# Performance work log

Measured on AMD Instinct MI355X. Metric: run time of the kernel, lower is better.

The kernel has to match this reference:

```python
import jax, jax.numpy as jnp
import numpy as np

D_MODEL = 1024
NUM_HEADS = 16
D_K = D_MODEL // NUM_HEADS


def setup_inputs() -> dict:
    key = jax.random.key(0)
    ks = jax.random.split(key, 11)
    B, S = 2, 2048
    s = 1.0 / np.sqrt(D_MODEL)
    inp = {
        'q': jax.random.normal(ks[0], (B, S, D_MODEL), jnp.float32),
        'k': jax.random.normal(ks[1], (B, S, D_MODEL), jnp.float32),
        'v': jax.random.normal(ks[2], (B, S, D_MODEL), jnp.float32),
        'w_q': jax.random.normal(ks[3], (D_MODEL, D_MODEL), jnp.float32) * s,
        'b_q': jnp.zeros((D_MODEL,), jnp.float32),
        'w_k': jax.random.normal(ks[4], (D_MODEL, D_MODEL), jnp.float32) * s,
        'b_k': jnp.zeros((D_MODEL,), jnp.float32),
        'w_v': jax.random.normal(ks[5], (D_MODEL, D_MODEL), jnp.float32) * s,
        'b_v': jnp.zeros((D_MODEL,), jnp.float32),
        'w_o': jax.random.normal(ks[6], (D_MODEL, D_MODEL), jnp.float32) * s,
        'b_o': jnp.zeros((D_MODEL,), jnp.float32),
    }
    return inp


def reference(q, k, v, w_q, b_q, w_k, b_k, w_v, b_v, w_o, b_o):
    B, S, _ = q.shape
    # linear projections (torch Linear: x @ W.T + b)
    def proj(x, w, b):
        y = x @ w.T + b
        # [B, S, D] -> [B, H, S, d_k]
        return y.reshape(B, -1, NUM_HEADS, D_K).transpose(0, 2, 1, 3)

    Q = proj(q, w_q, b_q)
    K = proj(k, w_k, b_k)
    V = proj(v, w_v, b_v)

    scale = 1.0 / np.sqrt(D_K).astype(np.float32)
    scores = jnp.einsum('bhqd,bhkd->bhqk', Q, K) * scale  # [B,H,S,S]
    weights = jax.nn.softmax(scores, axis=-1)
    # dropout is identity in eval mode
    x = jnp.einsum('bhqk,bhkd->bhqd', weights, V)
    x = x.transpose(0, 2, 1, 3).reshape(B, S, NUM_HEADS * D_K)
    return x @ w_o.T + b_o
```

## Files before the change

kernel.cpp:

```cpp
#include <hip/hip_runtime.h>

typedef __attribute__((ext_vector_type(8))) short short8;
typedef __attribute__((ext_vector_type(4))) float f32x4;

#define NHEADS 16
#define DK 64
#define SEQ 2048
#define DMODEL 1024

__device__ __forceinline__ unsigned short f2bf(float f) {
  union { float f; unsigned int u; } c; c.f = f;
  unsigned int u = c.u;
  return (unsigned short)((u + 0x7FFFu + ((u >> 16) & 1u)) >> 16);
}

__device__ __forceinline__ float exp2_hw(float x) {
  float y;
  asm("v_exp_f32 %0, %1" : "=v"(y) : "v"(x));
  return y;
}

__device__ __forceinline__ unsigned int cvtpk_bf16(float lo, float hi) {
  unsigned int r;
  asm("v_cvt_pk_bf16_f32 %0, %1, %2" : "=v"(r) : "v"(lo), "v"(hi));
  return r;
}

__device__ __forceinline__ short8 ldg16(const unsigned short* p) {
  return *reinterpret_cast<const short8*>(p);
}

__device__ __forceinline__ void gload_lds16(const unsigned short* g, unsigned short* l) {
  __builtin_amdgcn_global_load_lds(
      (const __attribute__((address_space(1))) unsigned int*)g,
      (__attribute__((address_space(3))) unsigned int*)l, 16, 0, 0);
}

struct CastPtrs {
  const float* s0; const float* s1; const float* s2; const float* s3;
  const float* s4; const float* s5; const float* s6;
  unsigned short* d0; unsigned short* d1; unsigned short* d2; unsigned short* d3;
  unsigned short* d4; unsigned short* d5; unsigned short* d6;
};

__global__ void cast_all(CastPtrs c) {
  const int b = blockIdx.x;
  const float* s; unsigned short* d; int off;
  if (b < 4096)        { s = c.s0; d = c.d0; off = b; }
  else if (b < 8192)   { s = c.s1; d = c.d1; off = b - 4096; }
  else if (b < 12288)  { s = c.s2; d = c.d2; off = b - 8192; }
  else if (b < 13312)  { s = c.s3; d = c.d3; off = b - 12288; }
  else if (b < 14336)  { s = c.s4; d = c.d4; off = b - 13312; }
  else if (b < 15360)  { s = c.s5; d = c.d5; off = b - 14336; }
  else                 { s = c.s6; d = c.d6; off = b - 15360; }
  const int i = off * 256 + threadIdx.x;
  float4 v = reinterpret_cast<const float4*>(s)[i];
  ushort4 o;
  o.x = f2bf(v.x); o.y = f2bf(v.y); o.z = f2bf(v.z); o.w = f2bf(v.w);
  reinterpret_cast<ushort4*>(d)[i] = o;
}

struct ProjPtrs {
  const unsigned short* A0; const unsigned short* A1; const unsigned short* A2;
  const unsigned short* W0; const unsigned short* W1; const unsigned short* W2;
  const float* bias0; const float* bias1; const float* bias2;
  unsigned short* dst0; unsigned short* dst1; unsigned short* dst2;
};

__global__ __launch_bounds__(256) void gemm_proj(ProjPtrs p) {
  __shared__ __align__(16) unsigned short S[24576];
  const int mode = blockIdx.z;
  const unsigned short* A = mode == 0 ? p.A0 : (mode == 1 ? p.A1 : p.A2);
  const unsigned short* W = mode == 0 ? p.W0 : (mode == 1 ? p.W1 : p.W2);
  const float* bias = mode == 0 ? p.bias0 : (mode == 1 ? p.bias1 : p.bias2);
  unsigned short* dst = mode == 0 ? p.dst0 : (mode == 1 ? p.dst1 : p.dst2);
  const int m0 = blockIdx.y * 128, n0 = blockIdx.x * 128;
  const int t = threadIdx.x, lane = t & 63, w = t >> 6;
  const int wr = w >> 1, wc = w & 1;
  const int lr = lane >> 4, lc = lane & 15;
  const unsigned short* a_src0 = A + (size_t)(m0 + (t >> 2)) * DMODEL + (t & 3) * 8;
  const unsigned short* a_src1 = a_src0 + (size_t)64 * DMODEL;
  const unsigned short* w_src0 = W + (size_t)(n0 + (t >> 2)) * DMODEL + (t & 3) * 8;
  const unsigned short* w_src1 = w_src0 + (size_t)64 * DMODEL;

  f32x4 acc[4][4] = {};

#define PSTAGE(s, bi) do { \
    gload_lds16(a_src0 + (s) * 32, S + (bi) * 4096 + t * 8); \
    gload_lds16(a_src1 + (s) * 32, S + (bi) * 4096 + 2048 + t * 8); \
    gload_lds16(w_src0 + (s) * 32, S + 12288 + (bi) * 4096 + t * 8); \
    gload_lds16(w_src1 + (s) * 32, S + 12288 + (bi) * 4096 + 2048 + t * 8); } while (0)

  auto compute = [&](const int bi) {
    const unsigned short* Ab = S + bi * 4096;
    const unsigned short* Bb = S + 12288 + bi * 4096;
    short8 a[4], b[4];
#pragma unroll
    for (int i = 0; i < 4; ++i) {
      a[i] = *reinterpret_cast<const short8*>(Ab + (wr * 64 + i * 16 + lc) * 32 + lr * 8);
      b[i] = *reinterpret_cast<const short8*>(Bb + (wc * 64 + i * 16 + lc) * 32 + lr * 8);
    }
#pragma unroll
    for (int mi = 0; mi < 4; ++mi)
#pragma unroll
      for (int ni = 0; ni < 4; ++ni)
        acc[mi][ni] = __builtin_amdgcn_mfma_f32_16x16x32_bf16(a[mi], b[ni], acc[mi][ni], 0, 0, 0);
  };

  PSTAGE(0, 0);
  PSTAGE(1, 1);
  for (int k = 0; k < 30; ++k) {
    PSTAGE(k + 2, (k + 2) % 3);
    asm volatile("s_waitcnt vmcnt(8)" ::: "memory");
    __builtin_amdgcn_s_barrier();
    __builtin_amdgcn_sched_barrier(0);
    compute(k % 3);
    __builtin_amdgcn_sched_barrier(0);
    __builtin_amdgcn_s_barrier();
    __builtin_amdgcn_sched_barrier(0);
  }
  asm volatile("s_waitcnt vmcnt(4)" ::: "memory");
  __builtin_amdgcn_s_barrier();
  __builtin_amdgcn_sched_barrier(0);
  compute(0);
  __builtin_amdgcn_sched_barrier(0);
  __builtin_amdgcn_s_barrier();
  __builtin_amdgcn_sched_barrier(0);
  asm volatile("s_waitcnt vmcnt(0)" ::: "memory");
  __builtin_amdgcn_s_barrier();
  __builtin_amdgcn_sched_barrier(0);
  compute(1);

  if (mode == 2) {
    __syncthreads();
    unsigned short* T = S + w * 4608;
    const int h = (n0 + wc * 64) >> 6;
    const int rb0 = m0 + wr * 64;
    const int bb = rb0 >> 11, s_base = rb0 & 2047;
#pragma unroll
    for (int mi = 0; mi < 4; ++mi) {
#pragma unroll
      for (int ni = 0; ni < 4; ++ni) {
        const float bv = bias[n0 + wc * 64 + ni * 16 + lc];
        uint2 pk;
        pk.x = cvtpk_bf16(acc[mi][ni][0] + bv, acc[mi][ni][1] + bv);
        pk.y = cvtpk_bf16(acc[mi][ni][2] + bv, acc[mi][ni][3] + bv);
        *reinterpret_cast<uint2*>(&T[(ni * 16 + lc) * 72 + mi * 16 + lr * 4]) = pk;
      }
    }
    __builtin_amdgcn_sched_barrier(0);
    unsigned short* dstb = dst + ((size_t)(bb * NHEADS + h) * 64) * 2048 + s_base;
#pragma unroll
    for (int i = 0; i < 8; ++i) {
      const int drow = i * 8 + (lane >> 3), scol = (lane & 7) * 8;
      const short8 val = *reinterpret_cast<const short8*>(&T[drow * 72 + scol]);
      *reinterpret_cast<short8*>(dstb + (size_t)drow * 2048 + scol) = val;
    }
  } else {
    const float sc = (mode == 0) ? 0.18033688f : 1.0f;
#pragma unroll
    for (int mi = 0; mi < 4; ++mi) {
#pragma unroll
      for (int ni = 0; ni < 4; ++ni) {
        const int cg = n0 + wc * 64 + ni * 16 + lc;
        const int rb = m0 + wr * 64 + mi * 16 + lr * 4;
        const float bv = bias[cg];
        const int h = cg >> 6, d = cg & 63;
#pragma unroll
        for (int j = 0; j < 4; ++j) {
          const int rg = rb + j;
          const int bb = rg >> 11, s = rg & 2047;
          dst[((size_t)(bb * NHEADS + h) * SEQ + s) * DK + d] = f2bf((acc[mi][ni][j] + bv) * sc);
        }
      }
    }
  }
}

__global__ __launch_bounds__(256) void gemm_out(const unsigned short* __restrict__ A,
                                                const unsigned short* __restrict__ W,
                                                const float* __restrict__ bias,
                                                float* __restrict__ out) {
  __shared__ __align__(16) unsigned short S[18432];
  const int m0 = blockIdx.y * 128, n0 = blockIdx.x * 64;
  const int t = threadIdx.x, lane = t & 63, w = t >> 6;
  const int wr = w >> 1, wc = w & 1;
  const int lr = lane >> 4, lc = lane & 15;
  const unsigned short* a_src0 = A + (size_t)(m0 + (t >> 2)) * DMODEL + (t & 3) * 8;
  const unsigned short* a_src1 = a_src0 + (size_t)64 * DMODEL;
  const unsigned short* w_src0 = W + (size_t)(n0 + (t >> 2)) * DMODEL + (t & 3) * 8;

  f32x4 acc[4][2] = {};

#define OSTAGE(s, bi) do { \
    gload_lds16(a_src0 + (s) * 32, S + (bi) * 4096 + t * 8); \
    gload_lds16(a_src1 + (s) * 32, S + (bi) * 4096 + 2048 + t * 8); \
    gload_lds16(w_src0 + (s) * 32, S + 12288 + (bi) * 2048 + t * 8); } while (0)

  auto compute = [&](const int bi) {
    const unsigned short* Ab = S + bi * 4096;
    const unsigned short* Bb = S + 12288 + bi * 2048;
    short8 a[4], b[2];
#pragma unroll
    for (int i = 0; i < 4; ++i)
      a[i] = *reinterpret_cast<const short8*>(Ab + (wr * 64 + i * 16 + lc) * 32 + lr * 8);
#pragma unroll
    for (int i = 0; i < 2; ++i)
      b[i] = *reinterpret_cast<const short8*>(Bb + (wc * 32 + i * 16 + lc) * 32 + lr * 8);
#pragma unroll
    for (int mi = 0; mi < 4; ++mi)
#pragma unroll
      for (int ni = 0; ni < 2; ++ni)
        acc[mi][ni] = __builtin_amdgcn_mfma_f32_16x16x32_bf16(a[mi], b[ni], acc[mi][ni], 0, 0, 0);
  };

  OSTAGE(0, 0);
  OSTAGE(1, 1);
  for (int k = 0; k < 30; ++k) {
    OSTAGE(k + 2, (k + 2) % 3);
    asm volatile("s_waitcnt vmcnt(6)" ::: "memory");
    __builtin_amdgcn_s_barrier();
    __builtin_amdgcn_sched_barrier(0);
    compute(k % 3);
    __builtin_amdgcn_sched_barrier(0);
    __builtin_amdgcn_s_barrier();
    __builtin_amdgcn_sched_barrier(0);
  }
  asm volatile("s_waitcnt vmcnt(3)" ::: "memory");
  __builtin_amdgcn_s_barrier();
  __builtin_amdgcn_sched_barrier(0);
  compute(0);
  __builtin_amdgcn_sched_barrier(0);
  __builtin_amdgcn_s_barrier();
  __builtin_amdgcn_sched_barrier(0);
  asm volatile("s_waitcnt vmcnt(0)" ::: "memory");
  __builtin_amdgcn_s_barrier();
  __builtin_amdgcn_sched_barrier(0);
  compute(1);

#pragma unroll
  for (int mi = 0; mi < 4; ++mi)
#pragma unroll
    for (int ni = 0; ni < 2; ++ni) {
      const int cg = n0 + wc * 32 + ni * 16 + lc;
      const int rb = m0 + wr * 64 + mi * 16 + lr * 4;
      const float bv = bias[cg];
#pragma unroll
      for (int j = 0; j < 4; ++j)
        out[(size_t)(rb + j) * DMODEL + cg] = acc[mi][ni][j] + bv;
    }
}

__global__ __launch_bounds__(256) void attn_fwd(const unsigned short* __restrict__ Qh,
                                                const unsigned short* __restrict__ Kh,
                                                const unsigned short* __restrict__ Vt,
                                                unsigned short* __restrict__ Oh) {
  __shared__ __align__(16) unsigned short Ktile[2][4096];
  __shared__ __align__(16) unsigned short Vtile[2][4096];
  __shared__ __align__(16) unsigned short P[4][32][76];
  const int t = threadIdx.x, w = t >> 6, lane = t & 63;
  const int bx = ((blockIdx.x & 7) << 6) | (blockIdx.x >> 3);
  const int bh = bx >> 4, qblk = bx & 15;
  const int q0 = qblk * 128 + w * 32;
  const unsigned short* Qp = Qh + (size_t)bh * SEQ * DK;
  const unsigned short* Kp = Kh + (size_t)bh * SEQ * DK;
  const unsigned short* Vp = Vt + (size_t)bh * DK * SEQ;
  const int r = lane & 15, g = lane >> 4;

  const short8 qa0 = ldg16(Qp + (size_t)(q0 + r) * DK + g * 8);
  const short8 qa1 = ldg16(Qp + (size_t)(q0 + r) * DK + 32 + g * 8);
  const short8 qb0 = ldg16(Qp + (size_t)(q0 + 16 + r) * DK + g * 8);
  const short8 qb1 = ldg16(Qp + (size_t)(q0 + 16 + r) * DK + 32 + g * 8);

  const int c0 = w * 64 + lane, c1 = c0 + 256;
  const int r0 = c0 >> 3, s0 = (c0 & 7) ^ (r0 & 7);
  const int r1 = c1 >> 3, s1 = (c1 & 7) ^ (r1 & 7);
  const unsigned short* ks0 = Kp + r0 * DK + s0 * 8;
  const unsigned short* ks1 = Kp + r1 * DK + s1 * 8;
  const unsigned short* vs0 = Vp + (size_t)r0 * SEQ + s0 * 8;
  const unsigned short* vs1 = Vp + (size_t)r1 * SEQ + s1 * 8;

  float mA = -1e30f, lA = 0.f, mB = -1e30f, lB = 0.f;
  f32x4 oA[4] = {}, oB[4] = {};

  const int sw0 = ((g ^ (r & 7)) << 3);
  const int sw1 = (((g + 4) ^ (r & 7)) << 3);
  char* prowA = (char*)&P[w][r][0];
  char* prowB = (char*)&P[w][16 + r][0];

  gload_lds16(ks0, &Ktile[0][w * 512]);
  gload_lds16(ks1, &Ktile[0][2048 + w * 512]);
  gload_lds16(vs0, &Vtile[0][w * 512]);
  gload_lds16(vs1, &Vtile[0][2048 + w * 512]);
  __syncthreads();

  int buf = 0;
  for (int kt = 0; kt < 32; ++kt) {
    if (kt < 31) {
      const int kvn = (kt + 1) * 64;
      gload_lds16(ks0 + kvn * DK, &Ktile[buf ^ 1][w * 512]);
      gload_lds16(ks1 + kvn * DK, &Ktile[buf ^ 1][2048 + w * 512]);
      gload_lds16(vs0 + kvn, &Vtile[buf ^ 1][w * 512]);
      gload_lds16(vs1 + kvn, &Vtile[buf ^ 1][2048 + w * 512]);
    }
    f32x4 sA[4] = {}, sB[4] = {};
    __builtin_amdgcn_s_setprio(1);
#pragma unroll
    for (int nt = 0; nt < 4; ++nt) {
      const short8 k0 = *reinterpret_cast<const short8*>(&Ktile[buf][(nt * 16 + r) * 64 + sw0]);
      const short8 k1 = *reinterpret_cast<const short8*>(&Ktile[buf][(nt * 16 + r) * 64 + sw1]);
      sA[nt] = __builtin_amdgcn_mfma_f32_16x16x32_bf16(k0, qa0, sA[nt], 0, 0, 0);
      sA[nt] = __builtin_amdgcn_mfma_f32_16x16x32_bf16(k1, qa1, sA[nt], 0, 0, 0);
      sB[nt] = __builtin_amdgcn_mfma_f32_16x16x32_bf16(k0, qb0, sB[nt], 0, 0, 0);
      sB[nt] = __builtin_amdgcn_mfma_f32_16x16x32_bf16(k1, qb1, sB[nt], 0, 0, 0);
    }
    __builtin_amdgcn_s_setprio(0);
    {
      f32x4 pm;
#pragma unroll
      for (int j = 0; j < 4; ++j)
        pm[j] = fmaxf(fmaxf(sA[0][j], sA[1][j]), fmaxf(sA[2][j], sA[3][j]));
      float pmax = fmaxf(fmaxf(pm[0], pm[1]), fmaxf(pm[2], pm[3]));
      pmax = fmaxf(pmax, __shfl_xor(pmax, 16));
      pmax = fmaxf(pmax, __shfl_xor(pmax, 32));
      if (!__all(pmax - mA <= 8.f)) {
        const float mn = fmaxf(mA, pmax);
        const float al = exp2_hw(mA - mn);
        mA = mn; lA *= al;
        float alj[4];
#pragma unroll
        for (int j = 0; j < 4; ++j) alj[j] = __shfl(al, 4 * g + j, 16);
#pragma unroll
        for (int nt = 0; nt < 4; ++nt)
#pragma unroll
          for (int j = 0; j < 4; ++j) oA[nt][j] *= alj[j];
      }
#pragma unroll
      for (int nt = 0; nt < 4; ++nt)
#pragma unroll
        for (int j = 0; j < 4; ++j) sA[nt][j] = exp2_hw(sA[nt][j] - mA);
      f32x4 s4;
#pragma unroll
      for (int j = 0; j < 4; ++j) s4[j] = (sA[0][j] + sA[1][j]) + (sA[2][j] + sA[3][j]);
      float sum = (s4[0] + s4[1]) + (s4[2] + s4[3]);
      sum += __shfl_xor(sum, 16);
      sum += __shfl_xor(sum, 32);
      lA += sum;
#pragma unroll
      for (int nt = 0; nt < 4; ++nt) {
        uint2 pk;
        pk.x = cvtpk_bf16(sA[nt][0], sA[nt][1]);
        pk.y = cvtpk_bf16(sA[nt][2], sA[nt][3]);
        *reinterpret_cast<uint2*>(prowA + nt * 32 + g * 8) = pk;
      }
    }
    {
      f32x4 pm;
#pragma unroll
      for (int j = 0; j < 4; ++j)
        pm[j] = fmaxf(fmaxf(sB[0][j], sB[1][j]), fmaxf(sB[2][j], sB[3][j]));
      float pmax = fmaxf(fmaxf(pm[0], pm[1]), fmaxf(pm[2], pm[3]));
      pmax = fmaxf(pmax, __shfl_xor(pmax, 16));
      pmax = fmaxf(pmax, __shfl_xor(pmax, 32));
      if (!__all(pmax - mB <= 8.f)) {
        const float mn = fmaxf(mB, pmax);
        const float al = exp2_hw(mB - mn);
        mB = mn; lB *= al;
        float alj[4];
#pragma unroll
        for (int j = 0; j < 4; ++j) alj[j] = __shfl(al, 4 * g + j, 16);
#pragma unroll
        for (int nt = 0; nt < 4; ++nt)
#pragma unroll
          for (int j = 0; j < 4; ++j) oB[nt][j] *= alj[j];
      }
#pragma unroll
      for (int nt = 0; nt < 4; ++nt)
#pragma unroll
        for (int j = 0; j < 4; ++j) sB[nt][j] = exp2_hw(sB[nt][j] - mB);
      f32x4 s4;
#pragma unroll
      for (int j = 0; j < 4; ++j) s4[j] = (sB[0][j] + sB[1][j]) + (sB[2][j] + sB[3][j]);
      float sum = (s4[0] + s4[1]) + (s4[2] + s4[3]);
      sum += __shfl_xor(sum, 16);
      sum += __shfl_xor(sum, 32);
      lB += sum;
#pragma unroll
      for (int nt = 0; nt < 4; ++nt) {
        uint2 pk;
        pk.x = cvtpk_bf16(sB[nt][0], sB[nt][1]);
        pk.y = cvtpk_bf16(sB[nt][2], sB[nt][3]);
        *reinterpret_cast<uint2*>(prowB + nt * 32 + g * 8) = pk;
      }
    }
    union { short8 v; unsigned long long q[2]; } pA0, pA1, pB0, pB1;
    pA0.q[0] = *reinterpret_cast<const unsigned long long*>(prowA + g * 16);
    pA0.q[1] = *reinterpret_cast<const unsigned long long*>(prowA + g * 16 + 8);
    pA1.q[0] = *reinterpret_cast<const unsigned long long*>(prowA + 64 + g * 16);
    pA1.q[1] = *reinterpret_cast<const unsigned long long*>(prowA + 64 + g * 16 + 8);
    pB0.q[0] = *reinterpret_cast<const unsigned long long*>(prowB + g * 16);
    pB0.q[1] = *reinterpret_cast<const unsigned long long*>(prowB + g * 16 + 8);
    pB1.q[0] = *reinterpret_cast<const unsigned long long*>(prowB + 64 + g * 16);
    pB1.q[1] = *reinterpret_cast<const unsigned long long*>(prowB + 64 + g * 16 + 8);
    __builtin_amdgcn_s_setprio(1);
#pragma unroll
    for (int nt = 0; nt < 4; ++nt) {
      const short8 v0 = *reinterpret_cast<const short8*>(&Vtile[buf][(nt * 16 + r) * 64 + sw0]);
      const short8 v1 = *reinterpret_cast<const short8*>(&Vtile[buf][(nt * 16 + r) * 64 + sw1]);
      oA[nt] = __builtin_amdgcn_mfma_f32_16x16x32_bf16(pA0.v, v0, oA[nt], 0, 0, 0);
      oA[nt] = __builtin_amdgcn_mfma_f32_16x16x32_bf16(pA1.v, v1, oA[nt], 0, 0, 0);
      oB[nt] = __builtin_amdgcn_mfma_f32_16x16x32_bf16(pB0.v, v0, oB[nt], 0, 0, 0);
      oB[nt] = __builtin_amdgcn_mfma_f32_16x16x32_bf16(pB1.v, v1, oB[nt], 0, 0, 0);
    }
    __builtin_amdgcn_s_setprio(0);
    __syncthreads();
    buf ^= 1;
  }

  const float invA = 1.f / lA, invB = 1.f / lB;
  float ivA[4], ivB[4];
#pragma unroll
  for (int j = 0; j < 4; ++j) {
    ivA[j] = __shfl(invA, 4 * g + j, 16);
    ivB[j] = __shfl(invB, 4 * g + j, 16);
  }
  const size_t ob = ((size_t)((bh >> 4) * SEQ + q0)) * DMODEL + (size_t)(bh & 15) * DK;
#pragma unroll
  for (int nt = 0; nt < 4; ++nt)
#pragma unroll
    for (int j = 0; j < 4; ++j) {
      Oh[ob + (size_t)(g * 4 + j) * DMODEL + nt * 16 + r] = f2bf(oA[nt][j] * ivA[j]);
      Oh[ob + (size_t)(16 + g * 4 + j) * DMODEL + nt * 16 + r] = f2bf(oB[nt][j] * ivB[j]);
    }
}

extern "C" void kernel_launch(void* const* d_in, const int* in_sizes, int n_in,
                              void* d_out, int out_size, void* d_ws, size_t ws_size,
                              hipStream_t stream) {
  const float* q   = (const float*)d_in[0];
  const float* k   = (const float*)d_in[1];
  const float* v   = (const float*)d_in[2];
  const float* w_q = (const float*)d_in[3];
  const float* b_q = (const float*)d_in[4];
  const float* w_k = (const float*)d_in[5];
  const float* b_k = (const float*)d_in[6];
  const float* w_v = (const float*)d_in[7];
  const float* b_v = (const float*)d_in[8];
  const float* w_o = (const float*)d_in[9];
  const float* b_o = (const float*)d_in[10];
  float* out = (float*)d_out;
  char* ws = (char*)d_ws;
  const size_t MB = (size_t)1 << 20;
  unsigned short* qc  = (unsigned short*)(ws + 0 * MB);
  unsigned short* kc  = (unsigned short*)(ws + 8 * MB);
  unsigned short* vc  = (unsigned short*)(ws + 16 * MB);
  unsigned short* wqc = (unsigned short*)(ws + 24 * MB);
  unsigned short* wkc = (unsigned short*)(ws + 26 * MB);
  unsigned short* wvc = (unsigned short*)(ws + 28 * MB);
  unsigned short* woc = (unsigned short*)(ws + 30 * MB);
  unsigned short* Qh  = (unsigned short*)(ws + 32 * MB);
  unsigned short* Kh  = (unsigned short*)(ws + 40 * MB);
  unsigned short* Vt  = (unsigned short*)(ws + 48 * MB);
  unsigned short* Oh  = (unsigned short*)(ws + 56 * MB);

  CastPtrs cp;
  cp.s0 = q; cp.s1 = k; cp.s2 = v; cp.s3 = w_q; cp.s4 = w_k; cp.s5 = w_v; cp.s6 = w_o;
  cp.d0 = qc; cp.d1 = kc; cp.d2 = vc; cp.d3 = wqc; cp.d4 = wkc; cp.d5 = wvc; cp.d6 = woc;
  cast_all<<<16384, 256, 0, stream>>>(cp);

  ProjPtrs p;
  p.A0 = qc; p.A1 = kc; p.A2 = vc;
  p.W0 = wqc; p.W1 = wkc; p.W2 = wvc;
  p.bias0 = b_q; p.bias1 = b_k; p.bias2 = b_v;
  p.dst0 = Qh; p.dst1 = Kh; p.dst2 = Vt;
  gemm_proj<<<dim3(8, 32, 3), 256, 0, stream>>>(p);

  attn_fwd<<<512, 256, 0, stream>>>(Qh, Kh, Vt, Oh);

  gemm_out<<<dim3(16, 32), 256, 0, stream>>>(Oh, woc, b_o, out);
}
```

Before: 240.5 us.

## Fuse fp32-to-bf16 casts into projection and output GEMM loads

Removes the standalone cast kernel and has the GEMMs load fp32 inputs and weights directly into registers, convert them to bf16 and store them to LDS. This cuts one launch and the write and reread of the bf16 copies. The cost is that the async direct-to-LDS triple-buffered pipeline becomes a register-staged double buffer with two full barriers per step. Each GEMM also converts the same tiles repeatedly across blocks and reads twice as many bytes per element.

```diff
diff --git a/kernel.cpp b/kernel.cpp
--- a/kernel.cpp
+++ b/kernel.cpp
@@ -36,64 +36,60 @@
       (__attribute__((address_space(3))) unsigned int*)l, 16, 0, 0);
 }
 
-struct CastPtrs {
-  const float* s0; const float* s1; const float* s2; const float* s3;
-  const float* s4; const float* s5; const float* s6;
-  unsigned short* d0; unsigned short* d1; unsigned short* d2; unsigned short* d3;
-  unsigned short* d4; unsigned short* d5; unsigned short* d6;
-};
-
-__global__ void cast_all(CastPtrs c) {
-  const int b = blockIdx.x;
-  const float* s; unsigned short* d; int off;
-  if (b < 4096)        { s = c.s0; d = c.d0; off = b; }
-  else if (b < 8192)   { s = c.s1; d = c.d1; off = b - 4096; }
-  else if (b < 12288)  { s = c.s2; d = c.d2; off = b - 8192; }
-  else if (b < 13312)  { s = c.s3; d = c.d3; off = b - 12288; }
-  else if (b < 14336)  { s = c.s4; d = c.d4; off = b - 13312; }
-  else if (b < 15360)  { s = c.s5; d = c.d5; off = b - 14336; }
-  else                 { s = c.s6; d = c.d6; off = b - 15360; }
-  const int i = off * 256 + threadIdx.x;
-  float4 v = reinterpret_cast<const float4*>(s)[i];
-  ushort4 o;
-  o.x = f2bf(v.x); o.y = f2bf(v.y); o.z = f2bf(v.z); o.w = f2bf(v.w);
-  reinterpret_cast<ushort4*>(d)[i] = o;
-}
-
 struct ProjPtrs {
-  const unsigned short* A0; const unsigned short* A1; const unsigned short* A2;
-  const unsigned short* W0; const unsigned short* W1; const unsigned short* W2;
+  const float* A0; const float* A1; const float* A2;
+  const float* W0; const float* W1; const float* W2;
   const float* bias0; const float* bias1; const float* bias2;
   unsigned short* dst0; unsigned short* dst1; unsigned short* dst2;
 };
 
 __global__ __launch_bounds__(256) void gemm_proj(ProjPtrs p) {
-  __shared__ __align__(16) unsigned short S[24576];
+  __shared__ __align__(16) unsigned short S[18432];
   const int mode = blockIdx.z;
-  const unsigned short* A = mode == 0 ? p.A0 : (mode == 1 ? p.A1 : p.A2);
-  const unsigned short* W = mode == 0 ? p.W0 : (mode == 1 ? p.W1 : p.W2);
+  const float* A = mode == 0 ? p.A0 : (mode == 1 ? p.A1 : p.A2);
+  const float* W = mode == 0 ? p.W0 : (mode == 1 ? p.W1 : p.W2);
   const float* bias = mode == 0 ? p.bias0 : (mode == 1 ? p.bias1 : p.bias2);
   unsigned short* dst = mode == 0 ? p.dst0 : (mode == 1 ? p.dst1 : p.dst2);
   const int m0 = blockIdx.y * 128, n0 = blockIdx.x * 128;
   const int t = threadIdx.x, lane = t & 63, w = t >> 6;
   const int wr = w >> 1, wc = w & 1;
   const int lr = lane >> 4, lc = lane & 15;
-  const unsigned short* a_src0 = A + (size_t)(m0 + (t >> 2)) * DMODEL + (t & 3) * 8;
-  const unsigned short* a_src1 = a_src0 + (size_t)64 * DMODEL;
-  const unsigned short* w_src0 = W + (size_t)(n0 + (t >> 2)) * DMODEL + (t & 3) * 8;
-  const unsigned short* w_src1 = w_src0 + (size_t)64 * DMODEL;
+  const float* a_src0 = A + (size_t)(m0 + (t >> 2)) * DMODEL + (t & 3) * 8;
+  const float* a_src1 = a_src0 + (size_t)64 * DMODEL;
+  const float* w_src0 = W + (size_t)(n0 + (t >> 2)) * DMODEL + (t & 3) * 8;
+  const float* w_src1 = w_src0 + (size_t)64 * DMODEL;
 
   f32x4 acc[4][4] = {};
-
-#define PSTAGE(s, bi) do { \
-    gload_lds16(a_src0 + (s) * 32, S + (bi) * 4096 + t * 8); \
-    gload_lds16(a_src1 + (s) * 32, S + (bi) * 4096 + 2048 + t * 8); \
-    gload_lds16(w_src0 + (s) * 32, S + 12288 + (bi) * 4096 + t * 8); \
-    gload_lds16(w_src1 + (s) * 32, S + 12288 + (bi) * 4096 + 2048 + t * 8); } while (0)
+  float4 ra0, ra1, ra2, ra3, rw0, rw1, rw2, rw3;
+
+#define PLOADR(kk) do { \
+    ra0 = *reinterpret_cast<const float4*>(a_src0 + (kk)); \
+    ra1 = *reinterpret_cast<const float4*>(a_src0 + (kk) + 4); \
+    ra2 = *reinterpret_cast<const float4*>(a_src1 + (kk)); \
+    ra3 = *reinterpret_cast<const float4*>(a_src1 + (kk) + 4); \
+    rw0 = *reinterpret_cast<const float4*>(w_src0 + (kk)); \
+    rw1 = *reinterpret_cast<const float4*>(w_src0 + (kk) + 4); \
+    rw2 = *reinterpret_cast<const float4*>(w_src1 + (kk)); \
+    rw3 = *reinterpret_cast<const float4*>(w_src1 + (kk) + 4); } while (0)
+
+#define PWRITER(bi) do { \
+    uint4 u; \
+    u.x = cvtpk_bf16(ra0.x, ra0.y); u.y = cvtpk_bf16(ra0.z, ra0.w); \
+    u.z = cvtpk_bf16(ra1.x, ra1.y); u.w = cvtpk_bf16(ra1.z, ra1.w); \
+    *reinterpret_cast<uint4*>(S + (bi) * 4096 + t * 8) = u; \
+    u.x = cvtpk_bf16(ra2.x, ra2.y); u.y = cvtpk_bf16(ra2.z, ra2.w); \
+    u.z = cvtpk_bf16(ra3.x, ra3.y); u.w = cvtpk_bf16(ra3.z, ra3.w); \
+    *reinterpret_cast<uint4*>(S + (bi) * 4096 + 2048 + t * 8) = u; \
+    u.x = cvtpk_bf16(rw0.x, rw0.y); u.y = cvtpk_bf16(rw0.z, rw0.w); \
+    u.z = cvtpk_bf16(rw1.x, rw1.y); u.w = cvtpk_bf16(rw1.z, rw1.w); \
+    *reinterpret_cast<uint4*>(S + 8192 + (bi) * 4096 + t * 8) = u; \
+    u.x = cvtpk_bf16(rw2.x, rw2.y); u.y = cvtpk_bf16(rw2.z, rw2.w); \
+    u.z = cvtpk_bf16(rw3.x, rw3.y); u.w = cvtpk_bf16(rw3.z, rw3.w); \
+    *reinterpret_cast<uint4*>(S + 8192 + (bi) * 4096 + 2048 + t * 8) = u; } while (0)
 
   auto compute = [&](const int bi) {
     const unsigned short* Ab = S + bi * 4096;
-    const unsigned short* Bb = S + 12288 + bi * 4096;
+    const unsigned short* Bb = S + 8192 + bi * 4096;
     short8 a[4], b[4];
 #pragma unroll
     for (int i = 0; i < 4; ++i) {
@@ -107,32 +103,21 @@
         acc[mi][ni] = __builtin_amdgcn_mfma_f32_16x16x32_bf16(a[mi], b[ni], acc[mi][ni], 0, 0, 0);
   };
 
-  PSTAGE(0, 0);
-  PSTAGE(1, 1);
-  for (int k = 0; k < 30; ++k) {
-    PSTAGE(k + 2, (k + 2) % 3);
-    asm volatile("s_waitcnt vmcnt(8)" ::: "memory");
-    __builtin_amdgcn_s_barrier();
+  PLOADR(0);
+  PWRITER(0);
+  __syncthreads();
+  int buf = 0;
+  for (int k0 = 0; k0 < DMODEL; k0 += 32) {
+    if (k0 < DMODEL - 32) PLOADR(k0 + 32);
     __builtin_amdgcn_sched_barrier(0);
-    compute(k % 3);
-    __builtin_amdgcn_sched_barrier(0);
-    __builtin_amdgcn_s_barrier();
-    __builtin_amdgcn_sched_barrier(0);
+    compute(buf);
+    __syncthreads();
+    if (k0 < DMODEL - 32) PWRITER(buf ^ 1);
+    __syncthreads();
+    buf ^= 1;
   }
-  asm volatile("s_waitcnt vmcnt(4)" ::: "memory");
-  __builtin_amdgcn_s_barrier();
-  __builtin_amdgcn_sched_barrier(0);
-  compute(0);
-  __builtin_amdgcn_sched_barrier(0);
-  __builtin_amdgcn_s_barrier();
-  __builtin_amdgcn_sched_barrier(0);
-  asm volatile("s_waitcnt vmcnt(0)" ::: "memory");
-  __builtin_amdgcn_s_barrier();
-  __builtin_amdgcn_sched_barrier(0);
-  compute(1);
 
   if (mode == 2) {
-    __syncthreads();
     unsigned short* T = S + w * 4608;
     const int h = (n0 + wc * 64) >> 6;
     const int rb0 = m0 + wr * 64;
@@ -178,28 +163,38 @@
 }
 
 __global__ __launch_bounds__(256) void gemm_out(const unsigned short* __restrict__ A,
-                                                const unsigned short* __restrict__ W,
+                                                const float* __restrict__ W,
                                                 const float* __restrict__ bias,
                                                 float* __restrict__ out) {
-  __shared__ __align__(16) unsigned short S[18432];
+  __shared__ __align__(16) unsigned short S[12288];
   const int m0 = blockIdx.y * 128, n0 = blockIdx.x * 64;
   const int t = threadIdx.x, lane = t & 63, w = t >> 6;
   const int wr = w >> 1, wc = w & 1;
   const int lr = lane >> 4, lc = lane & 15;
   const unsigned short* a_src0 = A + (size_t)(m0 + (t >> 2)) * DMODEL + (t & 3) * 8;
   const unsigned short* a_src1 = a_src0 + (size_t)64 * DMODEL;
-  const unsigned short* w_src0 = W + (size_t)(n0 + (t >> 2)) * DMODEL + (t & 3) * 8;
+  const float* w_src0 = W + (size_t)(n0 + (t >> 2)) * DMODEL + (t & 3) * 8;
 
   f32x4 acc[4][2] = {};
-
-#define OSTAGE(s, bi) do { \
-    gload_lds16(a_src0 + (s) * 32, S + (bi) * 4096 + t * 8); \
-    gload_lds16(a_src1 + (s) * 32, S + (bi) * 4096 + 2048 + t * 8); \
-    gload_lds16(w_src0 + (s) * 32, S + 12288 + (bi) * 2048 + t * 8); } while (0)
+  float4 rw0, rw1;
+
+#define OSTAGE_A(kk, bi) do { \
+    gload_lds16(a_src0 + (kk), S + (bi) * 4096 + t * 8); \
+    gload_lds16(a_src1 + (kk), S + (bi) * 4096 + 2048 + t * 8); } while (0)
+
+#define OLOADR(kk) do { \
+    rw0 = *reinterpret_cast<const float4*>(w_src0 + (kk)); \
+    rw1 = *reinterpret_cast<const float4*>(w_src0 + (kk) + 4); } while (0)
+
+#define OWRITER(bi) do { \
+    uint4 u; \
+    u.x = cvtpk_bf16(rw0.x, rw0.y); u.y = cvtpk_bf16(rw0.z, rw0.w); \
+    u.z = cvtpk_bf16(rw1.x, rw1.y); u.w = cvtpk_bf16(rw1.z, rw1.w); \
+    *reinterpret_cast<uint4*>(S + 8192 + (bi) * 2048 + t * 8) = u; } while (0)
 
   auto compute = [&](const int bi) {
     const unsigned short* Ab = S + bi * 4096;
-    const unsigned short* Bb = S + 12288 + bi * 2048;
+    const unsigned short* Bb = S + 8192 + bi * 2048;
     short8 a[4], b[2];
 #pragma unroll
     for (int i = 0; i < 4; ++i)
@@ -214,29 +209,23 @@
         acc[mi][ni] = __builtin_amdgcn_mfma_f32_16x16x32_bf16(a[mi], b[ni], acc[mi][ni], 0, 0, 0);
   };
 
-  OSTAGE(0, 0);
-  OSTAGE(1, 1);
-  for (int k = 0; k < 30; ++k) {
-    OSTAGE(k + 2, (k + 2) % 3);
-    asm volatile("s_waitcnt vmcnt(6)" ::: "memory");
-    __builtin_amdgcn_s_barrier();
+  OSTAGE_A(0, 0);
+  OLOADR(0);
+  OWRITER(0);
+  __syncthreads();
+  int buf = 0;
+  for (int k0 = 0; k0 < DMODEL; k0 += 32) {
+    if (k0 < DMODEL - 32) {
+      OSTAGE_A(k0 + 32, buf ^ 1);
+      OLOADR(k0 + 32);
+    }
     __builtin_amdgcn_sched_barrier(0);
-    compute(k % 3);
-    __builtin_amdgcn_sched_barrier(0);
-    __builtin_amdgcn_s_barrier();
-    __builtin_amdgcn_sched_barrier(0);
+    compute(buf);
+    __syncthreads();
+    if (k0 < DMODEL - 32) OWRITER(buf ^ 1);
+    __syncthreads();
+    buf ^= 1;
   }
-  asm volatile("s_waitcnt vmcnt(3)" ::: "memory");
-  __builtin_amdgcn_s_barrier();
-  __builtin_amdgcn_sched_barrier(0);
-  compute(0);
-  __builtin_amdgcn_sched_barrier(0);
-  __builtin_amdgcn_s_barrier();
-  __builtin_amdgcn_sched_barrier(0);
-  asm volatile("s_waitcnt vmcnt(0)" ::: "memory");
-  __builtin_amdgcn_s_barrier();
-  __builtin_amdgcn_sched_barrier(0);
-  compute(1);
 
 #pragma unroll
   for (int mi = 0; mi < 4; ++mi)
@@ -451,31 +440,19 @@
   float* out = (float*)d_out;
   char* ws = (char*)d_ws;
   const size_t MB = (size_t)1 << 20;
-  unsigned short* qc  = (unsigned short*)(ws + 0 * MB);
-  unsigned short* kc  = (unsigned short*)(ws + 8 * MB);
-  unsigned short* vc  = (unsigned short*)(ws + 16 * MB);
-  unsigned short* wqc = (unsigned short*)(ws + 24 * MB);
-  unsigned short* wkc = (unsigned short*)(ws + 26 * MB);
-  unsigned short* wvc = (unsigned short*)(ws + 28 * MB);
-  unsigned short* woc = (unsigned short*)(ws + 30 * MB);
   unsigned short* Qh  = (unsigned short*)(ws + 32 * MB);
   unsigned short* Kh  = (unsigned short*)(ws + 40 * MB);
   unsigned short* Vt  = (unsigned short*)(ws + 48 * MB);
   unsigned short* Oh  = (unsigned short*)(ws + 56 * MB);
 
-  CastPtrs cp;
-  cp.s0 = q; cp.s1 = k; cp.s2 = v; cp.s3 = w_q; cp.s4 = w_k; cp.s5 = w_v; cp.s6 = w_o;
-  cp.d0 = qc; cp.d1 = kc; cp.d2 = vc; cp.d3 = wqc; cp.d4 = wkc; cp.d5 = wvc; cp.d6 = woc;
-  cast_all<<<16384, 256, 0, stream>>>(cp);
-
   ProjPtrs p;
-  p.A0 = qc; p.A1 = kc; p.A2 = vc;
-  p.W0 = wqc; p.W1 = wkc; p.W2 = wvc;
+  p.A0 = q; p.A1 = k; p.A2 = v;
+  p.W0 = w_q; p.W1 = w_k; p.W2 = w_v;
   p.bias0 = b_q; p.bias1 = b_k; p.bias2 = b_v;
   p.dst0 = Qh; p.dst1 = Kh; p.dst2 = Vt;
   gemm_proj<<<dim3(8, 32, 3), 256, 0, stream>>>(p);
 
   attn_fwd<<<512, 256, 0, stream>>>(Qh, Kh, Vt, Oh);
 
-  gemm_out<<<dim3(16, 32), 256, 0, stream>>>(Oh, woc, b_o, out);
-}
+  gemm_out<<<dim3(16, 32), 256, 0, stream>>>(Oh, w_o, b_o, out);
+}
```

Measured after the change: 282.0 us. 17.3% more time.
